# Kernel optimization log

Measured on AMD Instinct MI355X. Metric: run time of the kernel, lower is better.

The kernel has to match this reference:

```python
import jax, jax.numpy as jnp
import numpy as np

B, S, D = 8, 4096, 256
H, DK, DV = 8, 32, 32


def _layer_norm(x, g, b, eps=1e-6):
    mu = jnp.mean(x, axis=-1, keepdims=True)
    var = jnp.mean(jnp.square(x - mu), axis=-1, keepdims=True)
    return (x - mu) * jax.lax.rsqrt(var + eps) * g + b


def setup_inputs() -> dict:
    key = jax.random.key(0)
    ks = jax.random.split(key, 16)
    std = 1.0 / np.sqrt(D)
    p = lambda k, shp: (jax.random.normal(k, shp, jnp.float32) * std)
    return {
        "h": jax.random.normal(ks[0], (B, S, D), jnp.float32),
        "e": jax.random.normal(ks[1], (B, S, D), jnp.float32),
        "s": jax.random.normal(ks[2], (B, D), jnp.float32),
        "sat_wq": p(ks[3], (D, H * DK)), "sat_wk": p(ks[4], (D, H * DK)),
        "sat_wv": p(ks[5], (D, H * DV)), "sat_wo": p(ks[6], (H * DV, D)),
        "sat_g": jnp.ones((D,), jnp.float32), "sat_b": jnp.zeros((D,), jnp.float32),
        "rel_wq": p(ks[7], (D, H * DK)), "rel_wk": p(ks[8], (D, H * DK)),
        "rel_wv": p(ks[9], (D, H * DV)), "rel_wo": p(ks[10], (H * DV, D)),
        "rel_g": jnp.ones((D,), jnp.float32), "rel_b": jnp.zeros((D,), jnp.float32),
    }


def reference(h, e, s, sat_wq, sat_wk, sat_wv, sat_wo, sat_g, sat_b,
              rel_wq, rel_wk, rel_wv, rel_wo, rel_g, rel_b):
    b, sl, d = h.shape
    scale = 1.0 / np.sqrt(DK)

    # ---- build 5-token context: [left, self, right, entity, relay] ----
    hp = jnp.pad(h, ((0, 0), (1, 1), (0, 0)))  # zeros at both ends
    s_exp = jnp.broadcast_to(s[:, None, :], (b, sl, d))
    ctx = jnp.stack([hp[:, :sl], h, hp[:, 2:], e, s_exp], axis=2)  # [B,S,5,D]

    # ---- satellite attention: 1 query vs 5-token context per position ----
    q = (h @ sat_wq).reshape(b, sl, H, DK)
    k = (ctx @ sat_wk).reshape(b, sl, 5, H, DK)
    v = (ctx @ sat_wv).reshape(b, sl, 5, H, DV)
    attn = jax.nn.softmax(jnp.einsum('bshd,bschd->bshc', q, k) * scale, axis=-1)
    o = jnp.einsum('bshc,bschd->bshd', attn, v).reshape(b, sl, H * DV) @ sat_wo
    h_out = _layer_norm(o + h, sat_g, sat_b)  # [B,S,D]

    # ---- relay attention: relay query vs [s; h_out] ----
    s_h = jnp.concatenate([s[:, None, :], h_out], axis=1)  # [B,S+1,D]
    qr = (s @ rel_wq).reshape(b, H, DK)
    kr = (s_h @ rel_wk).reshape(b, sl + 1, H, DK)
    vr = (s_h @ rel_wv).reshape(b, sl + 1, H, DV)
    attn_r = jax.nn.softmax(jnp.einsum('bhd,bkhd->bhk', qr, kr) * scale, axis=-1)
    orl = jnp.einsum('bhk,bkhd->bhd', attn_r, vr).reshape(b, H * DV) @ rel_wo
    s_out = _layer_norm(orl + s, rel_g, rel_b)  # [B,D]

    return (h_out, s_out)
```

## Files before the change

kernel.cpp:

```cpp
#include <hip/hip_runtime.h>
#include <hip/hip_bf16.h>

typedef unsigned short ushort_t;
typedef unsigned int uint_t;
typedef __attribute__((ext_vector_type(8))) short bf16x8;
typedef __attribute__((ext_vector_type(4))) float f32x4;

#define NB 8
#define NS 4096
#define ND 256
#define NH 8
#define NDK 32
#define NBS (NB*NS)
#define NK  (NS+1)
#define CH  513
#define NCH 8
static const size_t PBUF = (size_t)NB*(NS+1)*ND;
static const size_t HSZ  = (size_t)NBS*ND;

__device__ __forceinline__ ushort_t f2b(float x){
  union { __hip_bfloat16 b; ushort_t u; } cv; cv.b = __float2bfloat16(x); return cv.u;
}
__device__ __forceinline__ float b2f(ushort_t u){
  union { uint_t u; float f; } cv; cv.u = ((uint_t)u) << 16; return cv.f;
}
__device__ __forceinline__ void gload16(const ushort_t* g, ushort_t* l){
  __builtin_amdgcn_global_load_lds(
      (const __attribute__((address_space(1))) void*)g,
      (__attribute__((address_space(3))) void*)l, 16, 0, 0);
}

__device__ __forceinline__ float bsum256(float v){
  __shared__ float tmp[4];
  #pragma unroll
  for (int o=32;o>0;o>>=1) v += __shfl_down(v,o);
  if ((threadIdx.x & 63)==0) tmp[threadIdx.x>>6] = v;
  __syncthreads();
  float r = tmp[0]+tmp[1]+tmp[2]+tmp[3];
  __syncthreads();
  return r;
}

__global__ __launch_bounds__(256) void prep(
    const float* __restrict__ h, const float* __restrict__ e,
    ushort_t* __restrict__ h16, ushort_t* __restrict__ e16,
    const float* __restrict__ w0, const float* __restrict__ w1, const float* __restrict__ w2,
    const float* __restrict__ w3, const float* __restrict__ w4, const float* __restrict__ w5,
    ushort_t* __restrict__ WtAll,
    const float* __restrict__ s,
    const float* __restrict__ rwq,
    ushort_t* __restrict__ ksb, ushort_t* __restrict__ vsb,
    float* __restrict__ qr, ushort_t* __restrict__ krv)
{
  __shared__ float sh[64*68];
  const int blk = blockIdx.x;
  const int tid = threadIdx.x;
  if (blk < 8192){
    const float* X = (blk < 4096) ? h : e;
    ushort_t*    Y = (blk < 4096) ? h16 : e16;
    size_t i = ((size_t)(blk & 4095)*256 + tid)*8;
    float4 a = *(const float4*)(X+i), b = *(const float4*)(X+i+4);
    uint4 o;
    o.x = f2b(a.x) | ((uint_t)f2b(a.y)<<16);
    o.y = f2b(a.z) | ((uint_t)f2b(a.w)<<16);
    o.z = f2b(b.x) | ((uint_t)f2b(b.y)<<16);
    o.w = f2b(b.z) | ((uint_t)f2b(b.w)<<16);
    *(uint4*)(Y+i) = o;
  } else if (blk < 8288){
    const int idx = blk - 8192;
    const int z = idx >> 4, xy = idx & 15;
    const float* W = (z==0)?w0:(z==1)?w1:(z==2)?w2:(z==3)?w3:(z==4)?w4:w5;
    ushort_t* Wt = WtAll + (size_t)z*65536;
    float (*t)[68] = (float(*)[68])sh;
    const int k0 = (xy>>2)*64, n0 = (xy&3)*64;
    const int tr = tid>>4, tc4 = (tid&15)*4;
    #pragma unroll
    for (int i=0;i<4;i++){
      int r = tr + i*16;
      float4 v = *(const float4*)&W[(size_t)(k0+r)*ND + n0 + tc4];
      t[r][tc4]=v.x; t[r][tc4+1]=v.y; t[r][tc4+2]=v.z; t[r][tc4+3]=v.w;
    }
    __syncthreads();
    #pragma unroll
    for (int i=0;i<4;i++){
      int n = tr + i*16;
      uint_t q0 = f2b(t[tc4+0][n]) | ((uint_t)f2b(t[tc4+1][n])<<16);
      uint_t q1 = f2b(t[tc4+2][n]) | ((uint_t)f2b(t[tc4+3][n])<<16);
      *(uint2*)&Wt[(size_t)(n0+n)*ND + k0 + tc4] = make_uint2(q0,q1);
    }
  } else {
    const int rem = blk - 8288;
    const int b = rem & 7, which = rem >> 3;
    const float* W = (which==0)?w1:(which==1)?w2:(which==2)?rwq:(which==3)?w4:w5;
    float* a = sh;
    a[tid] = s[(size_t)b*ND + tid];
    __syncthreads();
    float acc = 0.f;
    #pragma unroll 8
    for (int d=0; d<ND; d++)
      acc = fmaf(a[d], W[(size_t)d*ND + tid], acc);
    switch (which){
      case 0: ksb[(size_t)b*ND + tid] = f2b(acc); break;
      case 1: vsb[(size_t)b*ND + tid] = f2b(acc); break;
      case 2: qr[(size_t)b*ND + tid] = acc; break;
      case 3: krv[(size_t)b*NK*512 + tid] = f2b(acc); break;
      default: krv[(size_t)b*NK*512 + 256 + tid] = f2b(acc); break;
    }
  }
}

__global__ __launch_bounds__(256) void gemm_qkve(const ushort_t* __restrict__ h16,
    const ushort_t* __restrict__ e16, const ushort_t* __restrict__ Wt,
    ushort_t* __restrict__ hQKV, ushort_t* __restrict__ eKV)
{
  __shared__ __align__(16) ushort_t As[2][128][64];
  __shared__ __align__(16) ushort_t Bs[2][128][64];
  const int y = blockIdx.y;
  const ushort_t* A; const ushort_t* Wb; ushort_t* Y; int ldn, col0;
  if (y < 6){ A=h16; Wb=Wt;        Y=hQKV; ldn=768; col0=y*128; }
  else      { A=e16; Wb=Wt+65536;  Y=eKV;  ldn=512; col0=(y-6)*128; }
  const int tid  = threadIdx.x;
  const int row0 = blockIdx.x*128;
  const int lane = tid & 63;
  const int wave = tid >> 6;
  const int wr = (wave>>1)*64, wc = (wave&1)*64;
  const int l15 = lane & 15, lg = lane >> 4;
  const int lr8 = lane >> 3;
  const int ls  = (lane & 7) ^ lr8;

  const ushort_t* Asrc = A  + (size_t)(row0 + wave*32 + lr8)*ND + ls*8;
  const ushort_t* Bsrc = Wb + (size_t)(col0 + wave*32 + lr8)*ND + ls*8;

  f32x4 acc[4][4] = {};

  #define STAGE(t, bb) do{ \
    _Pragma("unroll") \
    for (int i=0;i<4;i++){ \
      gload16(Asrc + (size_t)i*8*ND + (t)*64, &As[bb][wave*32+i*8][0]); \
      gload16(Bsrc + (size_t)i*8*ND + (t)*64, &Bs[bb][wave*32+i*8][0]); \
    } \
  }while(0)
  #define COMPUTE(bb) do{ \
    _Pragma("unroll") \
    for (int ks=0; ks<2; ks++){ \
      bf16x8 af[4], bfr[4]; \
      _Pragma("unroll") \
      for (int mi=0;mi<4;mi++){ \
        int ra = wr + mi*16 + l15; int cb = (ks<<6) + (lg<<4); \
        af[mi] = *(const bf16x8*)((const char*)&As[bb][0][0] + ra*128 + (cb ^ ((ra&7)<<4))); \
      } \
      _Pragma("unroll") \
      for (int ni=0;ni<4;ni++){ \
        int rb = wc + ni*16 + l15; int cb = (ks<<6) + (lg<<4); \
        bfr[ni] = *(const bf16x8*)((const char*)&Bs[bb][0][0] + rb*128 + (cb ^ ((rb&7)<<4))); \
      } \
      _Pragma("unroll") \
      for (int mi=0;mi<4;mi++) \
        _Pragma("unroll") \
        for (int ni=0;ni<4;ni++) \
          acc[mi][ni] = __builtin_amdgcn_mfma_f32_16x16x32_bf16(af[mi], bfr[ni], acc[mi][ni], 0,0,0); \
    } \
  }while(0)

  STAGE(0, 0);
  __syncthreads();
  STAGE(1, 1); COMPUTE(0); __syncthreads();
  STAGE(2, 0); COMPUTE(1); __syncthreads();
  STAGE(3, 1); COMPUTE(0); __syncthreads();
  COMPUTE(1);
  #undef STAGE
  #undef COMPUTE

  #pragma unroll
  for (int mi=0;mi<4;mi++)
    #pragma unroll
    for (int r=0;r<4;r++){
      size_t orow = (size_t)(row0 + wr + mi*16 + lg*4 + r);
      #pragma unroll
      for (int ni=0;ni<4;ni++)
        Y[orow*(size_t)ldn + col0 + wc + ni*16 + l15] = f2b(acc[mi][ni][r]);
    }
}

__global__ __launch_bounds__(256) void gemm_krv(const ushort_t* __restrict__ A,
    const ushort_t* __restrict__ Wt, ushort_t* __restrict__ Y)
{
  __shared__ __align__(16) ushort_t As[2][128][64];
  __shared__ __align__(16) ushort_t Bs[2][128][64];
  const int tid  = threadIdx.x;
  const int row0 = blockIdx.x*128;
  const int col0 = blockIdx.y*128;
  const int lane = tid & 63;
  const int wave = tid >> 6;
  const int wr = (wave>>1)*64, wc = (wave&1)*64;
  const int l15 = lane & 15, lg = lane >> 4;
  const int lr8 = lane >> 3;
  const int ls  = (lane & 7) ^ lr8;

  const ushort_t* Asrc = A  + (size_t)(row0 + wave*32 + lr8)*ND + ls*8;
  const ushort_t* Bsrc = Wt + (size_t)(col0 + wave*32 + lr8)*ND + ls*8;

  f32x4 acc[4][4] = {};

  #define STAGE(t, bb) do{ \
    _Pragma("unroll") \
    for (int i=0;i<4;i++){ \
      gload16(Asrc + (size_t)i*8*ND + (t)*64, &As[bb][wave*32+i*8][0]); \
      gload16(Bsrc + (size_t)i*8*ND + (t)*64, &Bs[bb][wave*32+i*8][0]); \
    } \
  }while(0)
  #define COMPUTE(bb) do{ \
    _Pragma("unroll") \
    for (int ks=0; ks<2; ks++){ \
      bf16x8 af[4], bfr[4]; \
      _Pragma("unroll") \
      for (int mi=0;mi<4;mi++){ \
        int ra = wr + mi*16 + l15; int cb = (ks<<6) + (lg<<4); \
        af[mi] = *(const bf16x8*)((const char*)&As[bb][0][0] + ra*128 + (cb ^ ((ra&7)<<4))); \
      } \
      _Pragma("unroll") \
      for (int ni=0;ni<4;ni++){ \
        int rb = wc + ni*16 + l15; int cb = (ks<<6) + (lg<<4); \
        bfr[ni] = *(const bf16x8*)((const char*)&Bs[bb][0][0] + rb*128 + (cb ^ ((rb&7)<<4))); \
      } \
      _Pragma("unroll") \
      for (int mi=0;mi<4;mi++) \
        _Pragma("unroll") \
        for (int ni=0;ni<4;ni++) \
          acc[mi][ni] = __builtin_amdgcn_mfma_f32_16x16x32_bf16(af[mi], bfr[ni], acc[mi][ni], 0,0,0); \
    } \
  }while(0)

  STAGE(0, 0);
  __syncthreads();
  STAGE(1, 1); COMPUTE(0); __syncthreads();
  STAGE(2, 0); COMPUTE(1); __syncthreads();
  STAGE(3, 1); COMPUTE(0); __syncthreads();
  COMPUTE(1);
  #undef STAGE
  #undef COMPUTE

  #pragma unroll
  for (int mi=0;mi<4;mi++)
    #pragma unroll
    for (int r=0;r<4;r++){
      int row = row0 + wr + mi*16 + lg*4 + r;
      size_t orow = (size_t)(row>>12)*NK + 1 + (row&4095);
      #pragma unroll
      for (int ni=0;ni<4;ni++)
        Y[orow*512 + col0 + wc + ni*16 + l15] = f2b(acc[mi][ni][r]);
    }
}

__global__ __launch_bounds__(256) void oproj_ln(const ushort_t* __restrict__ A,
    const ushort_t* __restrict__ Wt, const float* __restrict__ hres,
    const float* __restrict__ g, const float* __restrict__ bta,
    float* __restrict__ outf, ushort_t* __restrict__ outb)
{
  __shared__ __align__(16) ushort_t As[2][128][64];
  __shared__ __align__(16) ushort_t Bs[2][256][64];
  __shared__ float rs[128][2], rq[128][2];
  __shared__ float gl[ND], bl[ND];
  const int tid  = threadIdx.x;
  const int row0 = blockIdx.x*128;
  const int lane = tid & 63;
  const int wave = tid >> 6;
  const int wr = (wave>>1)*64, wc = (wave&1)*128;
  const int l15 = lane & 15, lg = lane >> 4;
  const int lr8 = lane >> 3;
  const int ls  = (lane & 7) ^ lr8;

  gl[tid] = g[tid]; bl[tid] = bta[tid];

  const ushort_t* Asrc = A  + (size_t)(row0 + wave*32 + lr8)*ND + ls*8;
  const ushort_t* Bsrc = Wt + (size_t)(wave*64 + lr8)*ND + ls*8;

  f32x4 acc[4][8] = {};

  #define STAGE2(t, bb) do{ \
    _Pragma("unroll") \
    for (int i=0;i<4;i++) \
      gload16(Asrc + (size_t)i*8*ND + (t)*64, &As[bb][wave*32+i*8][0]); \
    _Pragma("unroll") \
    for (int i=0;i<8;i++) \
      gload16(Bsrc + (size_t)i*8*ND + (t)*64, &Bs[bb][wave*64+i*8][0]); \
  }while(0)
  #define COMPUTE2(bb) do{ \
    _Pragma("unroll") \
    for (int ks=0; ks<2; ks++){ \
      bf16x8 af[4], bfr[8]; \
      _Pragma("unroll") \
      for (int mi=0;mi<4;mi++){ \
        int ra = wr + mi*16 + l15; int cb = (ks<<6) + (lg<<4); \
        af[mi] = *(const bf16x8*)((const char*)&As[bb][0][0] + ra*128 + (cb ^ ((ra&7)<<4))); \
      } \
      _Pragma("unroll") \
      for (int ni=0;ni<8;ni++){ \
        int rb = wc + ni*16 + l15; int cb = (ks<<6) + (lg<<4); \
        bfr[ni] = *(const bf16x8*)((const char*)&Bs[bb][0][0] + rb*128 + (cb ^ ((rb&7)<<4))); \
      } \
      _Pragma("unroll") \
      for (int mi=0;mi<4;mi++) \
        _Pragma("unroll") \
        for (int ni=0;ni<8;ni++) \
          acc[mi][ni] = __builtin_amdgcn_mfma_f32_16x16x32_bf16(af[mi], bfr[ni], acc[mi][ni], 0,0,0); \
    } \
  }while(0)

  STAGE2(0, 0);
  __syncthreads();
  STAGE2(1, 1); COMPUTE2(0); __syncthreads();
  STAGE2(2, 0); COMPUTE2(1); __syncthreads();
  STAGE2(3, 1); COMPUTE2(0); __syncthreads();
  COMPUTE2(1);
  #undef STAGE2
  #undef COMPUTE2

  #pragma unroll
  for (int mi=0;mi<4;mi++)
    #pragma unroll
    for (int rr=0;rr<4;rr++){
      size_t rowb = (size_t)(row0 + wr + mi*16 + lg*4 + rr)*ND;
      #pragma unroll
      for (int ni=0;ni<8;ni++)
        acc[mi][ni][rr] += hres[rowb + wc + ni*16 + l15];
    }

  #pragma unroll
  for (int mi=0;mi<4;mi++)
    #pragma unroll
    for (int rr=0;rr<4;rr++){
      float sv = 0.f, qv = 0.f;
      #pragma unroll
      for (int ni=0;ni<8;ni++){ float x = acc[mi][ni][rr]; sv += x; qv += x*x; }
      #pragma unroll
      for (int o=1;o<16;o<<=1){ sv += __shfl_xor(sv,o); qv += __shfl_xor(qv,o); }
      if (l15 == 0){
        int rl = wr + mi*16 + lg*4 + rr;
        rs[rl][wave&1] = sv; rq[rl][wave&1] = qv;
      }
    }
  __syncthreads();

  #pragma unroll
  for (int mi=0;mi<4;mi++)
    #pragma unroll
    for (int rr=0;rr<4;rr++){
      int rl = wr + mi*16 + lg*4 + rr;
      float sm = rs[rl][0] + rs[rl][1];
      float sq = rq[rl][0] + rq[rl][1];
      float mu = sm * (1.0f/ND);
      float var = sq * (1.0f/ND) - mu*mu;
      float rstd = rsqrtf(var + 1e-6f);
      size_t rowb = (size_t)(row0 + rl)*ND;
      #pragma unroll
      for (int ni=0;ni<8;ni++){
        int col = wc + ni*16 + l15;
        float yv = (acc[mi][ni][rr] - mu)*rstd*gl[col] + bl[col];
        outf[rowb + col] = yv;
        outb[rowb + col] = f2b(yv);
      }
    }
}

__device__ __forceinline__ void load8(float* d, const ushort_t* p){
  bf16x8 v = *(const bf16x8*)p;
  #pragma unroll
  for (int i=0;i<8;i++) d[i] = b2f((ushort_t)v[i]);
}
__device__ __forceinline__ void zero8(float* d){
  #pragma unroll
  for (int i=0;i<8;i++) d[i] = 0.f;
}
__global__ __launch_bounds__(256) void sat_attn4(const ushort_t* __restrict__ HQ,
    const ushort_t* __restrict__ EKV,
    const ushort_t* __restrict__ KS, const ushort_t* __restrict__ VS,
    ushort_t* __restrict__ O)
{
  const int tid = threadIdx.x;
  const int l  = tid & 3;
  const int g  = tid >> 2;
  const int hh = g & 7;
  const int pi = g >> 3;
  const int pos = blockIdx.x*8 + pi;
  const int b = pos >> 12, t = pos & 4095;
  const int co = hh*NDK + l*8;
  const float scale = 0.17677669529663687f;

  const size_t rq = (size_t)pos*768;
  const size_t re = (size_t)pos*512;
  float q[8], k0[8], k1[8], k2[8], k3[8], k4[8];
  load8(q,  HQ + rq + co);
  load8(k1, HQ + rq + 256 + co);
  load8(k3, EKV + re + co);
  load8(k4, KS + (size_t)b*ND + co);
  if (t > 0)    load8(k0, HQ + rq - 768 + 256 + co);
  else          zero8(k0);
  if (t < NS-1) load8(k2, HQ + rq + 768 + 256 + co);
  else          zero8(k2);

  float s0=0.f,s1=0.f,s2=0.f,s3=0.f,s4=0.f;
  #pragma unroll
  for (int i=0;i<8;i++){
    s0 = fmaf(q[i],k0[i],s0); s1 = fmaf(q[i],k1[i],s1); s2 = fmaf(q[i],k2[i],s2);
    s3 = fmaf(q[i],k3[i],s3); s4 = fmaf(q[i],k4[i],s4);
  }
  #pragma unroll
  for (int mm=1; mm<4; mm<<=1){
    s0 += __shfl_xor(s0,mm); s1 += __shfl_xor(s1,mm); s2 += __shfl_xor(s2,mm);
    s3 += __shfl_xor(s3,mm); s4 += __shfl_xor(s4,mm);
  }
  s0*=scale; s1*=scale; s2*=scale; s3*=scale; s4*=scale;
  float m = fmaxf(fmaxf(fmaxf(s0,s1),fmaxf(s2,s3)),s4);
  float p0=expf(s0-m), p1=expf(s1-m), p2=expf(s2-m), p3=expf(s3-m), p4=expf(s4-m);
  float inv = 1.0f/(p0+p1+p2+p3+p4);

  float v0[8], v1[8], v2[8], v3[8], v4[8];
  load8(v1, HQ + rq + 512 + co);
  load8(v3, EKV + re + 256 + co);
  load8(v4, VS + (size_t)b*ND + co);
  if (t > 0)    load8(v0, HQ + rq - 768 + 512 + co);
  else          zero8(v0);
  if (t < NS-1) load8(v2, HQ + rq + 768 + 512 + co);
  else          zero8(v2);

  float o[8];
  #pragma unroll
  for (int i=0;i<8;i++)
    o[i] = (p0*v0[i] + p1*v1[i] + p2*v2[i] + p3*v3[i] + p4*v4[i]) * inv;
  uint4 pk;
  pk.x = f2b(o[0])|((uint_t)f2b(o[1])<<16);
  pk.y = f2b(o[2])|((uint_t)f2b(o[3])<<16);
  pk.z = f2b(o[4])|((uint_t)f2b(o[5])<<16);
  pk.w = f2b(o[6])|((uint_t)f2b(o[7])<<16);
  *(uint4*)&O[(size_t)pos*ND + co] = pk;
}

__global__ __launch_bounds__(256) void rel_part(const float* __restrict__ QR,
    const ushort_t* __restrict__ KRV,
    float* __restrict__ pO, float* __restrict__ pM, float* __restrict__ pL)
{
  const int bh = blockIdx.x;
  const int b = bh >> 3, h = bh & 7;
  const int c = blockIdx.y;
  const int k0 = c*CH;
  const int kn = min(NK, k0+CH) - k0;
  const int tid = threadIdx.x;
  __shared__ float sc[CH];
  __shared__ float qs[NDK];
  __shared__ float red[8][NDK];
  __shared__ float tmp[4];
  if (tid < NDK) qs[tid] = QR[(size_t)b*ND + h*NDK + tid];
  __syncthreads();
  const float scale = 0.17677669529663687f;
  for (int kk=tid; kk<kn; kk+=256){
    const ushort_t* kp = KRV + ((size_t)b*NK + k0 + kk)*512 + h*NDK;
    float sdot = 0.f;
    #pragma unroll
    for (int w=0; w<4; w++){
      bf16x8 kv = *(const bf16x8*)(kp + w*8);
      #pragma unroll
      for (int i=0;i<8;i++) sdot = fmaf(qs[w*8+i], b2f((ushort_t)kv[i]), sdot);
    }
    sc[kk] = sdot * scale;
  }
  __syncthreads();
  float lm = -1e30f;
  for (int kk=tid; kk<kn; kk+=256) lm = fmaxf(lm, sc[kk]);
  #pragma unroll
  for (int o=32;o>0;o>>=1) lm = fmaxf(lm, __shfl_down(lm,o));
  if ((tid & 63)==0) tmp[tid>>6] = lm;
  __syncthreads();
  float m = fmaxf(fmaxf(tmp[0],tmp[1]),fmaxf(tmp[2],tmp[3]));
  __syncthreads();
  float ls = 0.f;
  for (int kk=tid; kk<kn; kk+=256){ float p = expf(sc[kk]-m); sc[kk] = p; ls += p; }
  #pragma unroll
  for (int o=32;o>0;o>>=1) ls += __shfl_down(ls,o);
  if ((tid & 63)==0) tmp[tid>>6] = ls;
  __syncthreads();
  float lsum = tmp[0]+tmp[1]+tmp[2]+tmp[3];
  int grp = tid>>5, d = tid&31;
  float acc = 0.f;
  for (int kk=grp; kk<kn; kk+=8)
    acc = fmaf(sc[kk], b2f(KRV[((size_t)b*NK + k0 + kk)*512 + 256 + h*NDK + d]), acc);
  red[grp][d] = acc;
  __syncthreads();
  if (grp == 0){
    float tot = 0.f;
    #pragma unroll
    for (int i=0;i<8;i++) tot += red[i][d];
    pO[((size_t)bh*NCH + c)*NDK + d] = tot;
    if (d == 0){ pM[bh*NCH + c] = m; pL[bh*NCH + c] = lsum; }
  }
}

__global__ __launch_bounds__(256) void rel_tail(const float* __restrict__ pO,
    const float* __restrict__ pM, const float* __restrict__ pL,
    const float* __restrict__ WO, const float* __restrict__ Sv,
    const float* __restrict__ g, const float* __restrict__ bta,
    float* __restrict__ out)
{
  const int b = blockIdx.x, j = threadIdx.x;
  __shared__ float ol[ND];
  {
    const int h = j >> 5, d = j & 31;
    const int bh = b*NH + h;
    float m = -1e30f;
    #pragma unroll
    for (int c=0;c<NCH;c++) m = fmaxf(m, pM[bh*NCH + c]);
    float o = 0.f, l = 0.f;
    #pragma unroll
    for (int c=0;c<NCH;c++){
      float w = expf(pM[bh*NCH + c] - m);
      o = fmaf(pO[((size_t)bh*NCH + c)*NDK + d], w, o);
      l = fmaf(pL[bh*NCH + c], w, l);
    }
    ol[j] = o / l;
  }
  __syncthreads();
  float x = 0.f;
  for (int d=0; d<ND; d++) x = fmaf(ol[d], WO[(size_t)d*ND + j], x);
  x += Sv[(size_t)b*ND + j];
  float mu = bsum256(x) * (1.0f/ND);
  float dd = x - mu;
  float var = bsum256(dd*dd) * (1.0f/ND);
  out[(size_t)NBS*ND + (size_t)b*ND + j] = dd * rsqrtf(var + 1e-6f) * g[j] + bta[j];
}

extern "C" void kernel_launch(void* const* d_in, const int* in_sizes, int n_in,
                              void* d_out, int out_size, void* d_ws, size_t ws_size,
                              hipStream_t stream)
{
  const float* h      = (const float*)d_in[0];
  const float* e      = (const float*)d_in[1];
  const float* s      = (const float*)d_in[2];
  const float* sat_wq = (const float*)d_in[3];
  const float* sat_wk = (const float*)d_in[4];
  const float* sat_wv = (const float*)d_in[5];
  const float* sat_wo = (const float*)d_in[6];
  const float* sat_g  = (const float*)d_in[7];
  const float* sat_b  = (const float*)d_in[8];
  const float* rel_wq = (const float*)d_in[9];
  const float* rel_wk = (const float*)d_in[10];
  const float* rel_wv = (const float*)d_in[11];
  const float* rel_wo = (const float*)d_in[12];
  const float* rel_g  = (const float*)d_in[13];
  const float* rel_b  = (const float*)d_in[14];
  float* out = (float*)d_out;

  float* ws = (float*)d_ws;
  ushort_t* hQKV = (ushort_t*)ws;
  ushort_t* h16  = (ushort_t*)(ws + (3*PBUF)/2);
  ushort_t* eKV  = (ushort_t*)(ws + 2*PBUF);
  ushort_t* krv  = (ushort_t*)(ws + 4*PBUF);
  ushort_t* hb   = (ushort_t*)(ws + 5*PBUF);
  ushort_t* satO = hb + HSZ;
  ushort_t* e16  = satO + HSZ;
  ushort_t* Wt   = e16 + HSZ;
  float* smalls  = (float*)(Wt + 6*65536);
  ushort_t* ksb = (ushort_t*)smalls;
  ushort_t* vsb = ksb + 2048;
  float* qr  = smalls + 4096;
  float* pO  = smalls + 8192;
  float* pM  = pO + (size_t)NB*NH*NCH*NDK;
  float* pL  = pM + NB*NH*NCH;

  dim3 gb(256);

  prep<<<8328, gb, 0, stream>>>(h, e, h16, e16,
      sat_wq, sat_wk, sat_wv, sat_wo, rel_wk, rel_wv, Wt,
      s, rel_wq, ksb, vsb, qr, krv);

  gemm_qkve<<<dim3(NBS/128, 10), gb, 0, stream>>>(h16, e16, Wt, hQKV, eKV);

  sat_attn4<<<NBS/8, gb, 0, stream>>>(hQKV, eKV, ksb, vsb, satO);

  oproj_ln<<<NBS/128, gb, 0, stream>>>(satO, Wt + 3*65536, h, sat_g, sat_b, out, hb);

  gemm_krv<<<dim3(NBS/128, 4), gb, 0, stream>>>(hb, Wt + 4*65536, krv);

  rel_part<<<dim3(NB*NH, NCH), gb, 0, stream>>>(qr, krv, pO, pM, pL);

  rel_tail<<<NB, gb, 0, stream>>>(pO, pM, pL, rel_wo, s, rel_g, rel_b, out);
}
```

Measured before the change: 175.2 us.

## Widen oproj_ln to 512 threads and read weights directly from global

The output-projection plus layernorm kernel now runs 8 waves per block instead of 4, each wave owning a 64x64 tile, so per-thread accumulators halve. Weight fragments are loaded straight from global/L2 into registers, and the shared-memory staging of the weight tile is dropped, cutting LDS use and allowing more resident blocks. The cost is repeated global weight reads across blocks and wave rows with no LDS reuse, plus a four-way row-statistics reduction.

```diff
diff --git a/kernel.cpp b/kernel.cpp
--- a/kernel.cpp
+++ b/kernel.cpp
@@ -252,69 +252,62 @@
     }
 }
 
-__global__ __launch_bounds__(256) void oproj_ln(const ushort_t* __restrict__ A,
+__global__ __launch_bounds__(512) void oproj_ln(const ushort_t* __restrict__ A,
     const ushort_t* __restrict__ Wt, const float* __restrict__ hres,
     const float* __restrict__ g, const float* __restrict__ bta,
     float* __restrict__ outf, ushort_t* __restrict__ outb)
 {
   __shared__ __align__(16) ushort_t As[2][128][64];
-  __shared__ __align__(16) ushort_t Bs[2][256][64];
-  __shared__ float rs[128][2], rq[128][2];
+  __shared__ float rs[128][4], rq[128][4];
   __shared__ float gl[ND], bl[ND];
   const int tid  = threadIdx.x;
   const int row0 = blockIdx.x*128;
   const int lane = tid & 63;
   const int wave = tid >> 6;
-  const int wr = (wave>>1)*64, wc = (wave&1)*128;
+  const int wr = (wave>>2)*64;
+  const int wc = (wave&3)*64;
   const int l15 = lane & 15, lg = lane >> 4;
   const int lr8 = lane >> 3;
   const int ls  = (lane & 7) ^ lr8;
 
-  gl[tid] = g[tid]; bl[tid] = bta[tid];
-
-  const ushort_t* Asrc = A  + (size_t)(row0 + wave*32 + lr8)*ND + ls*8;
-  const ushort_t* Bsrc = Wt + (size_t)(wave*64 + lr8)*ND + ls*8;
-
-  f32x4 acc[4][8] = {};
-
-  #define STAGE2(t, bb) do{ \
-    _Pragma("unroll") \
-    for (int i=0;i<4;i++) \
-      gload16(Asrc + (size_t)i*8*ND + (t)*64, &As[bb][wave*32+i*8][0]); \
-    _Pragma("unroll") \
-    for (int i=0;i<8;i++) \
-      gload16(Bsrc + (size_t)i*8*ND + (t)*64, &Bs[bb][wave*64+i*8][0]); \
+  if (tid < ND){ gl[tid] = g[tid]; bl[tid] = bta[tid]; }
+
+  const ushort_t* Asrc = A + (size_t)(row0 + wave*8 + lr8)*ND + ls*8;
+
+  f32x4 acc[4][4] = {};
+
+  #define STAGE3(t, bb) do{ \
+    gload16(Asrc + (t)*64,                 &As[bb][wave*8][0]); \
+    gload16(Asrc + (size_t)64*ND + (t)*64, &As[bb][wave*8+64][0]); \
   }while(0)
-  #define COMPUTE2(bb) do{ \
+  #define COMPUTE3(t, bb) do{ \
     _Pragma("unroll") \
     for (int ks=0; ks<2; ks++){ \
-      bf16x8 af[4], bfr[8]; \
+      bf16x8 af[4], bfr[4]; \
       _Pragma("unroll") \
       for (int mi=0;mi<4;mi++){ \
         int ra = wr + mi*16 + l15; int cb = (ks<<6) + (lg<<4); \
         af[mi] = *(const bf16x8*)((const char*)&As[bb][0][0] + ra*128 + (cb ^ ((ra&7)<<4))); \
       } \
       _Pragma("unroll") \
-      for (int ni=0;ni<8;ni++){ \
-        int rb = wc + ni*16 + l15; int cb = (ks<<6) + (lg<<4); \
-        bfr[ni] = *(const bf16x8*)((const char*)&Bs[bb][0][0] + rb*128 + (cb ^ ((rb&7)<<4))); \
-      } \
+      for (int ni=0;ni<4;ni++) \
+        bfr[ni] = *(const bf16x8*)&Wt[(size_t)(wc + ni*16 + l15)*ND + (t)*64 + ks*32 + lg*8]; \
       _Pragma("unroll") \
       for (int mi=0;mi<4;mi++) \
         _Pragma("unroll") \
-        for (int ni=0;ni<8;ni++) \
+        for (int ni=0;ni<4;ni++) \
           acc[mi][ni] = __builtin_amdgcn_mfma_f32_16x16x32_bf16(af[mi], bfr[ni], acc[mi][ni], 0,0,0); \
     } \
   }while(0)
 
-  STAGE2(0, 0);
-  __syncthreads();
-  STAGE2(1, 1); COMPUTE2(0); __syncthreads();
-  STAGE2(2, 0); COMPUTE2(1); __syncthreads();
-  STAGE2(3, 1); COMPUTE2(0); __syncthreads();
-  COMPUTE2(1);
-  #undef STAGE2
-  #undef COMPUTE2
+  STAGE3(0, 0);
+  __syncthreads();
+  STAGE3(1, 1); COMPUTE3(0, 0); __syncthreads();
+  STAGE3(2, 0); COMPUTE3(1, 1); __syncthreads();
+  STAGE3(3, 1); COMPUTE3(2, 0); __syncthreads();
+  COMPUTE3(3, 1);
+  #undef STAGE3
+  #undef COMPUTE3
 
   #pragma unroll
   for (int mi=0;mi<4;mi++)
@@ -322,7 +315,7 @@
     for (int rr=0;rr<4;rr++){
       size_t rowb = (size_t)(row0 + wr + mi*16 + lg*4 + rr)*ND;
       #pragma unroll
-      for (int ni=0;ni<8;ni++)
+      for (int ni=0;ni<4;ni++)
         acc[mi][ni][rr] += hres[rowb + wc + ni*16 + l15];
     }
 
@@ -332,12 +325,12 @@
     for (int rr=0;rr<4;rr++){
       float sv = 0.f, qv = 0.f;
       #pragma unroll
-      for (int ni=0;ni<8;ni++){ float x = acc[mi][ni][rr]; sv += x; qv += x*x; }
+      for (int ni=0;ni<4;ni++){ float x = acc[mi][ni][rr]; sv += x; qv += x*x; }
       #pragma unroll
       for (int o=1;o<16;o<<=1){ sv += __shfl_xor(sv,o); qv += __shfl_xor(qv,o); }
       if (l15 == 0){
         int rl = wr + mi*16 + lg*4 + rr;
-        rs[rl][wave&1] = sv; rq[rl][wave&1] = qv;
+        rs[rl][wave&3] = sv; rq[rl][wave&3] = qv;
       }
     }
   __syncthreads();
@@ -347,14 +340,14 @@
     #pragma unroll
     for (int rr=0;rr<4;rr++){
       int rl = wr + mi*16 + lg*4 + rr;
-      float sm = rs[rl][0] + rs[rl][1];
-      float sq = rq[rl][0] + rq[rl][1];
+      float sm = rs[rl][0] + rs[rl][1] + rs[rl][2] + rs[rl][3];
+      float sq = rq[rl][0] + rq[rl][1] + rq[rl][2] + rq[rl][3];
       float mu = sm * (1.0f/ND);
       float var = sq * (1.0f/ND) - mu*mu;
       float rstd = rsqrtf(var + 1e-6f);
       size_t rowb = (size_t)(row0 + rl)*ND;
       #pragma unroll
-      for (int ni=0;ni<8;ni++){
+      for (int ni=0;ni<4;ni++){
         int col = wc + ni*16 + l15;
         float yv = (acc[mi][ni][rr] - mu)*rstd*gl[col] + bl[col];
         outf[rowb + col] = yv;
@@ -576,7 +569,7 @@
 
   sat_attn4<<<NBS/8, gb, 0, stream>>>(hQKV, eKV, ksb, vsb, satO);
 
-  oproj_ln<<<NBS/128, gb, 0, stream>>>(satO, Wt + 3*65536, h, sat_g, sat_b, out, hb);
+  oproj_ln<<<NBS/128, dim3(512), 0, stream>>>(satO, Wt + 3*65536, h, sat_g, sat_b, out, hb);
 
   gemm_krv<<<dim3(NBS/128, 4), gb, 0, stream>>>(hb, Wt + 4*65536, krv);
 
```

Result: no change. 177.2 us (+1.1%).
